# Kernel tuning notes

Measured on AMD Instinct MI355X. Metric: run time of the kernel, lower is better.

The kernel has to match this reference:

```python
import jax, jax.numpy as jnp
import numpy as np

EMBED = 512
HEADS = 8
HEAD_DIM = EMBED // HEADS
LN_EPS = 1e-5


def setup_inputs() -> dict:
    key = jax.random.key(0)
    ks = jax.random.split(key, 13)
    B, L = 4, 2048
    s = 1.0 / np.sqrt(EMBED)
    inp = {
        "values": jax.random.normal(ks[0], (B, L, EMBED), dtype=jnp.float32),
        "keys": jax.random.normal(ks[1], (B, L, EMBED), dtype=jnp.float32),
        "query": jax.random.normal(ks[2], (B, L, EMBED), dtype=jnp.float32),
        "Wq": jax.random.uniform(ks[3], (EMBED, EMBED), jnp.float32, -s, s),
        "bq": jax.random.uniform(ks[4], (EMBED,), jnp.float32, -s, s),
        "Wk": jax.random.uniform(ks[5], (EMBED, EMBED), jnp.float32, -s, s),
        "bk": jax.random.uniform(ks[6], (EMBED,), jnp.float32, -s, s),
        "Wv": jax.random.uniform(ks[7], (EMBED, EMBED), jnp.float32, -s, s),
        "bv": jax.random.uniform(ks[8], (EMBED,), jnp.float32, -s, s),
        "Wo": jax.random.uniform(ks[9], (EMBED, EMBED), jnp.float32, -s, s),
        "bo": jax.random.uniform(ks[10], (EMBED,), jnp.float32, -s, s),
        "ln_g": jnp.ones((EMBED,), jnp.float32),
        "ln_b": jnp.zeros((EMBED,), jnp.float32),
    }
    return inp


def reference(values, keys, query, Wq, bq, Wk, bk, Wv, bv, Wo, bo, ln_g, ln_b):
    B, L, _ = query.shape
    # separate QKV linears (torch Linear: x @ W^T + b)
    Q = (query @ Wq.T + bq).reshape(B, L, HEADS, HEAD_DIM)
    K = (keys @ Wk.T + bk).reshape(B, L, HEADS, HEAD_DIM)
    V = (values @ Wv.T + bv).reshape(B, L, HEADS, HEAD_DIM)
    # explicit QK^T scores: [B, H, Q, K]
    scores = jnp.einsum("nqhd,nkhd->nhqk", Q, K) / np.sqrt(HEAD_DIM)
    attn = jax.nn.softmax(scores, axis=-1)
    out = jnp.einsum("nhqk,nkhd->nqhd", attn, V).reshape(B, L, EMBED)
    out = out @ Wo.T + bo
    # residual + LayerNorm (dropout = identity in eval)
    x = out + query
    mu = jnp.mean(x, axis=-1, keepdims=True)
    var = jnp.var(x, axis=-1, keepdims=True)
    return (x - mu) * jax.lax.rsqrt(var + LN_EPS) * ln_g + ln_b
```

## Files before the change

kernel.cpp:

```cpp
#include <hip/hip_runtime.h>

typedef short bf16x8 __attribute__((ext_vector_type(8)));
typedef short s16x4 __attribute__((ext_vector_type(4)));
typedef float f32x4 __attribute__((ext_vector_type(4)));
typedef unsigned int uint4v __attribute__((ext_vector_type(4)));
typedef unsigned int uint2v __attribute__((ext_vector_type(2)));

#define BLM   8192
#define EMB   512
#define LSEQ  2048
#define NHEAD 8
#define HDIM  64

typedef __attribute__((address_space(3))) char lds_ch;

__device__ __forceinline__ unsigned short f2bf(float x) {
    unsigned int u = __builtin_bit_cast(unsigned int, x);
    u += 0x7FFFu + ((u >> 16) & 1u);
    return (unsigned short)(u >> 16);
}

__device__ __forceinline__ unsigned int cvtpk(float lo, float hi) {
    unsigned int r;
    asm("v_cvt_pk_bf16_f32 %0, %1, %2" : "=v"(r) : "v"(lo), "v"(hi));
    return r;
}

__device__ __forceinline__ int swz(int row, int bcol) {
    return row * 128 + (bcol ^ ((row & 7) << 4));
}

#define GLL16(g, l) __builtin_amdgcn_global_load_lds( \
    (const __attribute__((address_space(1))) void*)(g), \
    (__attribute__((address_space(3))) void*)(l), 16, 0, 0)

#define TR16(dst, a, OFF) asm volatile("ds_read_b64_tr_b16 %0, %1 offset:%2" \
    : "=v"(dst) : "v"(a), "n"(OFF))

__global__ __launch_bounds__(256, 3) void k_gemm_qkv(
    const float* __restrict__ Xq, const float* __restrict__ Xk, const float* __restrict__ Xv,
    const float* __restrict__ Wq, const float* __restrict__ Wk, const float* __restrict__ Wv,
    const float* __restrict__ bq, const float* __restrict__ bk, const float* __restrict__ bv,
    unsigned short* __restrict__ Qb, unsigned short* __restrict__ Kb, unsigned short* __restrict__ Vb)
{
    const int z = blockIdx.z;
    const float* X    = (z == 0) ? Xq : (z == 1) ? Xk : Xv;
    const float* W    = (z == 0) ? Wq : (z == 1) ? Wk : Wv;
    const float* bias = (z == 0) ? bq : (z == 1) ? bk : bv;
    unsigned short* out = (z == 0) ? Qb : (z == 1) ? Kb : Vb;
    const float osc = (z == 0) ? 0.125f * 1.44269504088896340736f : 1.0f;

    __shared__ __align__(16) char lds[32768];
    char* As = lds;
    char* Bs = lds + 16384;

    const int tid  = threadIdx.x;
    const int lane = tid & 63;
    const int wave = tid >> 6;
    const int wm = wave >> 1, wn = wave & 1;
    const int lr = lane & 15, lk = lane >> 4;
    const int m0 = blockIdx.x * 128, n0 = blockIdx.y * 128;

    f32x4 acc[4][4] = {};

    const float* pa = X + (size_t)(m0 + (tid >> 4)) * EMB + (tid & 15) * 4;
    const float* pb = W + (size_t)(n0 + (tid >> 4)) * EMB + (tid & 15) * 4;

    float4 ar[8], br[8];
    #pragma unroll
    for (int i = 0; i < 8; ++i) {
        ar[i] = *(const float4*)(pa + (size_t)i * 16 * EMB);
        br[i] = *(const float4*)(pb + (size_t)i * 16 * EMB);
    }
    pa += 64; pb += 64;

    for (int kt = 0; kt < 8; ++kt) {
        __syncthreads();
        #pragma unroll
        for (int i = 0; i < 8; ++i) {
            int f = tid + i * 256;
            int r = f >> 4, c4 = f & 15;
            uint2v p; p.x = cvtpk(ar[i].x, ar[i].y); p.y = cvtpk(ar[i].z, ar[i].w);
            *(uint2v*)(As + swz(r, c4 * 8)) = p;
            uint2v q; q.x = cvtpk(br[i].x, br[i].y); q.y = cvtpk(br[i].z, br[i].w);
            *(uint2v*)(Bs + swz(r, c4 * 8)) = q;
        }
        if (kt < 7) {
            #pragma unroll
            for (int i = 0; i < 8; ++i) {
                ar[i] = *(const float4*)(pa + (size_t)i * 16 * EMB);
                br[i] = *(const float4*)(pb + (size_t)i * 16 * EMB);
            }
            pa += 64; pb += 64;
        }
        __syncthreads();
        #pragma unroll
        for (int ks = 0; ks < 2; ++ks) {
            bf16x8 af[4], bfr[4];
            #pragma unroll
            for (int fm = 0; fm < 4; ++fm)
                af[fm] = *(const bf16x8*)(As + swz(wm * 64 + fm * 16 + lr, ks * 64 + lk * 16));
            #pragma unroll
            for (int fn = 0; fn < 4; ++fn)
                bfr[fn] = *(const bf16x8*)(Bs + swz(wn * 64 + fn * 16 + lr, ks * 64 + lk * 16));
            #pragma unroll
            for (int fm = 0; fm < 4; ++fm)
                #pragma unroll
                for (int fn = 0; fn < 4; ++fn)
                    acc[fm][fn] = __builtin_amdgcn_mfma_f32_16x16x32_bf16(af[fm], bfr[fn], acc[fm][fn], 0, 0, 0);
        }
    }
    #pragma unroll
    for (int fn = 0; fn < 4; ++fn) {
        int n = n0 + wn * 64 + fn * 16 + lr;
        float bv_ = bias[n];
        #pragma unroll
        for (int fm = 0; fm < 4; ++fm) {
            int mb = m0 + wm * 64 + fm * 16 + lk * 4;
            #pragma unroll
            for (int j = 0; j < 4; ++j)
                out[(size_t)(mb + j) * EMB + n] = f2bf((acc[fm][fn][j] + bv_) * osc);
        }
    }
}

__global__ __launch_bounds__(256, 3) void k_gemm_out(
    const unsigned short* __restrict__ AO, const float* __restrict__ Wo,
    const float* __restrict__ bo, const float* __restrict__ res,
    float* __restrict__ Xout)
{
    __shared__ __align__(16) char lds[32768];
    char* As = lds;
    char* Bs = lds + 16384;

    const int tid  = threadIdx.x;
    const int lane = tid & 63;
    const int wave = tid >> 6;
    const int wm = wave >> 1, wn = wave & 1;
    const int lr = lane & 15, lk = lane >> 4;
    const int m0 = blockIdx.x * 128, n0 = blockIdx.y * 128;

    f32x4 acc[4][4] = {};

    const unsigned short* pA = AO + (size_t)(m0 + (tid >> 3)) * EMB + (tid & 7) * 8;
    const float* pB = Wo + (size_t)(n0 + (tid >> 4)) * EMB + (tid & 15) * 4;

    uint4v arA[4]; float4 brB[8];
    #pragma unroll
    for (int i = 0; i < 4; ++i) arA[i] = *(const uint4v*)(pA + (size_t)i * 32 * EMB);
    #pragma unroll
    for (int i = 0; i < 8; ++i) brB[i] = *(const float4*)(pB + (size_t)i * 16 * EMB);
    pA += 64; pB += 64;

    for (int kt = 0; kt < 8; ++kt) {
        __syncthreads();
        #pragma unroll
        for (int i = 0; i < 4; ++i) {
            int f = tid + i * 256;
            int r = f >> 3, c8 = f & 7;
            *(uint4v*)(As + swz(r, c8 * 16)) = arA[i];
        }
        #pragma unroll
        for (int i = 0; i < 8; ++i) {
            int f = tid + i * 256;
            int r = f >> 4, c4 = f & 15;
            uint2v q; q.x = cvtpk(brB[i].x, brB[i].y); q.y = cvtpk(brB[i].z, brB[i].w);
            *(uint2v*)(Bs + swz(r, c4 * 8)) = q;
        }
        if (kt < 7) {
            #pragma unroll
            for (int i = 0; i < 4; ++i) arA[i] = *(const uint4v*)(pA + (size_t)i * 32 * EMB);
            #pragma unroll
            for (int i = 0; i < 8; ++i) brB[i] = *(const float4*)(pB + (size_t)i * 16 * EMB);
            pA += 64; pB += 64;
        }
        __syncthreads();
        #pragma unroll
        for (int ks = 0; ks < 2; ++ks) {
            bf16x8 af[4], bfr[4];
            #pragma unroll
            for (int fm = 0; fm < 4; ++fm)
                af[fm] = *(const bf16x8*)(As + swz(wm * 64 + fm * 16 + lr, ks * 64 + lk * 16));
            #pragma unroll
            for (int fn = 0; fn < 4; ++fn)
                bfr[fn] = *(const bf16x8*)(Bs + swz(wn * 64 + fn * 16 + lr, ks * 64 + lk * 16));
            #pragma unroll
            for (int fm = 0; fm < 4; ++fm)
                #pragma unroll
                for (int fn = 0; fn < 4; ++fn)
                    acc[fm][fn] = __builtin_amdgcn_mfma_f32_16x16x32_bf16(af[fm], bfr[fn], acc[fm][fn], 0, 0, 0);
        }
    }
    #pragma unroll
    for (int fn = 0; fn < 4; ++fn) {
        int n = n0 + wn * 64 + fn * 16 + lr;
        float bv_ = bo[n];
        #pragma unroll
        for (int fm = 0; fm < 4; ++fm) {
            int mb = m0 + wm * 64 + fm * 16 + lk * 4;
            #pragma unroll
            for (int j = 0; j < 4; ++j) {
                size_t idx = (size_t)(mb + j) * EMB + n;
                Xout[idx] = acc[fm][fn][j] + bv_ + res[idx];
            }
        }
    }
}

__global__ __launch_bounds__(256, 4) void k_attn(
    const unsigned short* __restrict__ Qb, const unsigned short* __restrict__ Kb,
    const unsigned short* __restrict__ Vb, unsigned short* __restrict__ AO)
{
    __shared__ __align__(16) char lds[32768];
    lds_ch* LB = (lds_ch*)lds;

    const int tid  = threadIdx.x;
    const int lane = tid & 63;
    const int wave = tid >> 6;
    const int lr = lane & 15, lk = lane >> 4;

    const int bid  = blockIdx.x;
    const int orig = (bid & 7) * 64 + (bid >> 3);
    const int qx = orig & 15, bh = orig >> 4;
    const int b = bh >> 3, h = bh & 7;
    const size_t base = (size_t)b * LSEQ * EMB + h * HDIM;
    const int q0 = qx * 128 + wave * 32;

    const int c0 = tid, c1 = tid + 256;
    auto kcol = [](int c) { int r = c >> 3; return ((c & 7) * 8) ^ ((r & 7) * 8); };
    const unsigned short* srcK0 = Kb + base + (size_t)(c0 >> 3) * EMB + kcol(c0);
    const unsigned short* srcK1 = Kb + base + (size_t)(c1 >> 3) * EMB + kcol(c1);
    auto vsrc = [&](int c) {
        int kv = ((c >> 3) & 15) * 4 + ((c >> 1) & 3);
        int d  = (c >> 7) * 16 + (c & 1) * 8;
        return Vb + base + (size_t)kv * EMB + d;
    };
    const unsigned short* srcV0 = vsrc(c0);
    const unsigned short* srcV1 = vsrc(c1);

    auto stage = [&](int par) {
        lds_ch* kd = LB + par * 8192 + wave * 1024;
        lds_ch* vd = LB + 16384 + par * 8192 + wave * 1024;
        GLL16(srcK0, kd);
        GLL16(srcK1, kd + 4096);
        GLL16(srcV0, vd);
        GLL16(srcV1, vd + 4096);
        srcK0 += 64 * EMB; srcK1 += 64 * EMB;
        srcV0 += 64 * EMB; srcV1 += 64 * EMB;
    };

    bf16x8 qf[2][2];
    #pragma unroll
    for (int qg = 0; qg < 2; ++qg)
        #pragma unroll
        for (int ks = 0; ks < 2; ++ks)
            qf[qg][ks] = *(const bf16x8*)(Qb + base + (size_t)(q0 + qg * 16 + lr) * EMB + ks * 32 + lk * 8);

    f32x4 oaccT[2][4] = {};
    float lrow[2] = {0.f, 0.f};

    lds_ch* vadB = LB + 16384 + lk * 128 + lr * 2;

    stage(0);

    for (int t = 0; t < 32; ++t) {
        const int par = t & 1;
        __syncthreads();
        if (t < 31) stage(par ^ 1);

        char* Kl = lds + par * 8192;
        f32x4 s0[4] = {}, s1[4] = {};
        __builtin_amdgcn_s_setprio(1);
        #pragma unroll
        for (int ks = 0; ks < 2; ++ks) {
            bf16x8 kf[4];
            #pragma unroll
            for (int blk = 0; blk < 4; ++blk)
                kf[blk] = *(const bf16x8*)(Kl + swz(blk * 16 + lr, ks * 64 + lk * 16));
            #pragma unroll
            for (int blk = 0; blk < 4; ++blk) {
                s0[blk] = __builtin_amdgcn_mfma_f32_16x16x32_bf16(kf[blk], qf[0][ks], s0[blk], 0, 0, 0);
                s1[blk] = __builtin_amdgcn_mfma_f32_16x16x32_bf16(kf[blk], qf[1][ks], s1[blk], 0, 0, 0);
            }
        }
        __builtin_amdgcn_s_setprio(0);

        #pragma unroll
        for (int blk = 0; blk < 4; ++blk)
            #pragma unroll
            for (int j = 0; j < 4; ++j) {
                s0[blk][j] = __builtin_amdgcn_exp2f(s0[blk][j]);
                s1[blk][j] = __builtin_amdgcn_exp2f(s1[blk][j]);
            }
        {
            f32x4 pc = (s0[0] + s0[1]) + (s0[2] + s0[3]);
            lrow[0] += (pc[0] + pc[1]) + (pc[2] + pc[3]);
            f32x4 qc = (s1[0] + s1[1]) + (s1[2] + s1[3]);
            lrow[1] += (qc[0] + qc[1]) + (qc[2] + qc[3]);
        }

        bf16x8 pf0[2], pf1[2];
        #pragma unroll
        for (int k = 0; k < 2; ++k) {
            uint4v w;
            w.x = cvtpk(s0[2 * k][0],     s0[2 * k][1]);
            w.y = cvtpk(s0[2 * k][2],     s0[2 * k][3]);
            w.z = cvtpk(s0[2 * k + 1][0], s0[2 * k + 1][1]);
            w.w = cvtpk(s0[2 * k + 1][2], s0[2 * k + 1][3]);
            pf0[k] = __builtin_bit_cast(bf16x8, w);
            uint4v v;
            v.x = cvtpk(s1[2 * k][0],     s1[2 * k][1]);
            v.y = cvtpk(s1[2 * k][2],     s1[2 * k][3]);
            v.z = cvtpk(s1[2 * k + 1][0], s1[2 * k + 1][1]);
            v.w = cvtpk(s1[2 * k + 1][2], s1[2 * k + 1][3]);
            pf1[k] = __builtin_bit_cast(bf16x8, v);
        }

        lds_ch* vad = vadB + par * 8192;
        __builtin_amdgcn_s_setprio(1);
        #pragma unroll
        for (int fd = 0; fd < 4; ++fd) {
            uint2v t0, t1, t2, t3;
            TR16(t0, vad, 0);    TR16(t1, vad, 512);
            TR16(t2, vad, 1024); TR16(t3, vad, 1536);
            asm volatile("s_waitcnt lgkmcnt(0)" ::: "memory");
            __builtin_amdgcn_sched_barrier(0);
            uint4v w0; w0.x = t0.x; w0.y = t0.y; w0.z = t1.x; w0.w = t1.y;
            uint4v w1; w1.x = t2.x; w1.y = t2.y; w1.z = t3.x; w1.w = t3.y;
            bf16x8 v0 = __builtin_bit_cast(bf16x8, w0);
            bf16x8 v1 = __builtin_bit_cast(bf16x8, w1);
            oaccT[0][fd] = __builtin_amdgcn_mfma_f32_16x16x32_bf16(v0, pf0[0], oaccT[0][fd], 0, 0, 0);
            oaccT[1][fd] = __builtin_amdgcn_mfma_f32_16x16x32_bf16(v0, pf1[0], oaccT[1][fd], 0, 0, 0);
            oaccT[0][fd] = __builtin_amdgcn_mfma_f32_16x16x32_bf16(v1, pf0[1], oaccT[0][fd], 0, 0, 0);
            oaccT[1][fd] = __builtin_amdgcn_mfma_f32_16x16x32_bf16(v1, pf1[1], oaccT[1][fd], 0, 0, 0);
            vad += 2048;
        }
        __builtin_amdgcn_s_setprio(0);
    }

    #pragma unroll
    for (int qg = 0; qg < 2; ++qg) {
        float lr_ = lrow[qg];
        lr_ += __shfl_xor(lr_, 16);
        lr_ += __shfl_xor(lr_, 32);
        float inv = 1.f / lr_;
        unsigned short* aorow = AO + base + (size_t)(q0 + qg * 16 + lr) * EMB;
        #pragma unroll
        for (int fd = 0; fd < 4; ++fd) {
            s16x4 s;
            #pragma unroll
            for (int j = 0; j < 4; ++j) s[j] = (short)f2bf(oaccT[qg][fd][j] * inv);
            *(s16x4*)(aorow + fd * 16 + lk * 4) = s;
        }
    }
}

__global__ __launch_bounds__(64) void k_ln(
    const float* __restrict__ X, const float* __restrict__ g,
    const float* __restrict__ bta, float* __restrict__ out)
{
    const int row = blockIdx.x, lane = threadIdx.x;
    const float* x = X + (size_t)row * EMB;
    float4 a = *(const float4*)(x + lane * 8);
    float4 c = *(const float4*)(x + lane * 8 + 4);
    float s  = a.x + a.y + a.z + a.w + c.x + c.y + c.z + c.w;
    float sq = a.x*a.x + a.y*a.y + a.z*a.z + a.w*a.w + c.x*c.x + c.y*c.y + c.z*c.z + c.w*c.w;
    #pragma unroll
    for (int msk = 1; msk < 64; msk <<= 1) { s += __shfl_xor(s, msk); sq += __shfl_xor(sq, msk); }
    float mu  = s * (1.f / 512.f);
    float var = sq * (1.f / 512.f) - mu * mu;
    float rs  = rsqrtf(var + 1e-5f);
    float4 g0 = *(const float4*)(g + lane * 8), g1 = *(const float4*)(g + lane * 8 + 4);
    float4 b0 = *(const float4*)(bta + lane * 8), b1 = *(const float4*)(bta + lane * 8 + 4);
    float4 o0, o1;
    o0.x = (a.x - mu) * rs * g0.x + b0.x;  o0.y = (a.y - mu) * rs * g0.y + b0.y;
    o0.z = (a.z - mu) * rs * g0.z + b0.z;  o0.w = (a.w - mu) * rs * g0.w + b0.w;
    o1.x = (c.x - mu) * rs * g1.x + b1.x;  o1.y = (c.y - mu) * rs * g1.y + b1.y;
    o1.z = (c.z - mu) * rs * g1.z + b1.z;  o1.w = (c.w - mu) * rs * g1.w + b1.w;
    *(float4*)(out + (size_t)row * EMB + lane * 8) = o0;
    *(float4*)(out + (size_t)row * EMB + lane * 8 + 4) = o1;
}

extern "C" void kernel_launch(void* const* d_in, const int* in_sizes, int n_in,
                              void* d_out, int out_size, void* d_ws, size_t ws_size,
                              hipStream_t stream) {
    const float* values = (const float*)d_in[0];
    const float* keys   = (const float*)d_in[1];
    const float* query  = (const float*)d_in[2];
    const float* Wq = (const float*)d_in[3];  const float* bq = (const float*)d_in[4];
    const float* Wk = (const float*)d_in[5];  const float* bk = (const float*)d_in[6];
    const float* Wv = (const float*)d_in[7];  const float* bv = (const float*)d_in[8];
    const float* Wo = (const float*)d_in[9];  const float* bo = (const float*)d_in[10];
    const float* lng = (const float*)d_in[11];
    const float* lnb = (const float*)d_in[12];

    char* ws = (char*)d_ws;
    unsigned short* Qb = (unsigned short*)(ws);
    unsigned short* Kb = (unsigned short*)(ws + 8u  * 1024 * 1024);
    unsigned short* Vb = (unsigned short*)(ws + 16u * 1024 * 1024);
    unsigned short* AO = (unsigned short*)(ws + 24u * 1024 * 1024);
    float*          Xr = (float*)(ws);

    dim3 gqkv(64, 4, 3);
    k_gemm_qkv<<<gqkv, 256, 0, stream>>>(query, keys, values, Wq, Wk, Wv, bq, bk, bv, Qb, Kb, Vb);
    k_attn<<<512, 256, 0, stream>>>(Qb, Kb, Vb, AO);
    k_gemm_out<<<dim3(64, 4), 256, 0, stream>>>(AO, Wo, bo, query, Xr);
    k_ln<<<8192, 64, 0, stream>>>(Xr, lng, lnb, (float*)d_out);
}
```

Baseline: 88.11 us.

## Split KV tile across wave pairs in attention and reduce partials via LDS

```diff
diff --git a/kernel.cpp b/kernel.cpp
--- a/kernel.cpp
+++ b/kernel.cpp
@@ -13,6 +13,7 @@
 #define HDIM  64
 
 typedef __attribute__((address_space(3))) char lds_ch;
+typedef __attribute__((address_space(3))) float lds_f32;
 
 __device__ __forceinline__ unsigned short f2bf(float x) {
     unsigned int u = __builtin_bit_cast(unsigned int, x);
@@ -217,14 +218,16 @@
     const int tid  = threadIdx.x;
     const int lane = tid & 63;
     const int wave = tid >> 6;
+    const int qh   = wave & 1;
+    const int kvh  = wave >> 1;
     const int lr = lane & 15, lk = lane >> 4;
 
     const int bid  = blockIdx.x;
-    const int orig = (bid & 7) * 64 + (bid >> 3);
-    const int qx = orig & 15, bh = orig >> 4;
+    const int orig = (bid & 7) * 128 + (bid >> 3);
+    const int qx = orig & 31, bh = orig >> 5;
     const int b = bh >> 3, h = bh & 7;
     const size_t base = (size_t)b * LSEQ * EMB + h * HDIM;
-    const int q0 = qx * 128 + wave * 32;
+    const int q0 = qx * 64 + qh * 32;
 
     const int c0 = tid, c1 = tid + 256;
     auto kcol = [](int c) { int r = c >> 3; return ((c & 7) * 8) ^ ((r & 7) * 8); };
@@ -259,7 +262,7 @@
     f32x4 oaccT[2][4] = {};
     float lrow[2] = {0.f, 0.f};
 
-    lds_ch* vadB = LB + 16384 + lk * 128 + lr * 2;
+    lds_ch* vadB = LB + 16384 + kvh * 1024 + lk * 128 + lr * 2;
 
     stage(0);
 
@@ -269,88 +272,98 @@
         if (t < 31) stage(par ^ 1);
 
         char* Kl = lds + par * 8192;
-        f32x4 s0[4] = {}, s1[4] = {};
+        f32x4 s0[2] = {}, s1[2] = {};
         __builtin_amdgcn_s_setprio(1);
         #pragma unroll
         for (int ks = 0; ks < 2; ++ks) {
-            bf16x8 kf[4];
-            #pragma unroll
-            for (int blk = 0; blk < 4; ++blk)
-                kf[blk] = *(const bf16x8*)(Kl + swz(blk * 16 + lr, ks * 64 + lk * 16));
-            #pragma unroll
-            for (int blk = 0; blk < 4; ++blk) {
-                s0[blk] = __builtin_amdgcn_mfma_f32_16x16x32_bf16(kf[blk], qf[0][ks], s0[blk], 0, 0, 0);
-                s1[blk] = __builtin_amdgcn_mfma_f32_16x16x32_bf16(kf[blk], qf[1][ks], s1[blk], 0, 0, 0);
-            }
+            bf16x8 kf0 = *(const bf16x8*)(Kl + swz((kvh * 2 + 0) * 16 + lr, ks * 64 + lk * 16));
+            bf16x8 kf1 = *(const bf16x8*)(Kl + swz((kvh * 2 + 1) * 16 + lr, ks * 64 + lk * 16));
+            s0[0] = __builtin_amdgcn_mfma_f32_16x16x32_bf16(kf0, qf[0][ks], s0[0], 0, 0, 0);
+            s1[0] = __builtin_amdgcn_mfma_f32_16x16x32_bf16(kf0, qf[1][ks], s1[0], 0, 0, 0);
+            s0[1] = __builtin_amdgcn_mfma_f32_16x16x32_bf16(kf1, qf[0][ks], s0[1], 0, 0, 0);
+            s1[1] = __builtin_amdgcn_mfma_f32_16x16x32_bf16(kf1, qf[1][ks], s1[1], 0, 0, 0);
         }
         __builtin_amdgcn_s_setprio(0);
 
         #pragma unroll
-        for (int blk = 0; blk < 4; ++blk)
+        for (int blk = 0; blk < 2; ++blk)
             #pragma unroll
             for (int j = 0; j < 4; ++j) {
                 s0[blk][j] = __builtin_amdgcn_exp2f(s0[blk][j]);
                 s1[blk][j] = __builtin_amdgcn_exp2f(s1[blk][j]);
             }
         {
-            f32x4 pc = (s0[0] + s0[1]) + (s0[2] + s0[3]);
+            f32x4 pc = s0[0] + s0[1];
             lrow[0] += (pc[0] + pc[1]) + (pc[2] + pc[3]);
-            f32x4 qc = (s1[0] + s1[1]) + (s1[2] + s1[3]);
+            f32x4 qc = s1[0] + s1[1];
             lrow[1] += (qc[0] + qc[1]) + (qc[2] + qc[3]);
         }
 
-        bf16x8 pf0[2], pf1[2];
-        #pragma unroll
-        for (int k = 0; k < 2; ++k) {
-            uint4v w;
-            w.x = cvtpk(s0[2 * k][0],     s0[2 * k][1]);
-            w.y = cvtpk(s0[2 * k][2],     s0[2 * k][3]);
-            w.z = cvtpk(s0[2 * k + 1][0], s0[2 * k + 1][1]);
-            w.w = cvtpk(s0[2 * k + 1][2], s0[2 * k + 1][3]);
-            pf0[k] = __builtin_bit_cast(bf16x8, w);
-            uint4v v;
-            v.x = cvtpk(s1[2 * k][0],     s1[2 * k][1]);
-            v.y = cvtpk(s1[2 * k][2],     s1[2 * k][3]);
-            v.z = cvtpk(s1[2 * k + 1][0], s1[2 * k + 1][1]);
-            v.w = cvtpk(s1[2 * k + 1][2], s1[2 * k + 1][3]);
-            pf1[k] = __builtin_bit_cast(bf16x8, v);
-        }
+        uint4v w;
+        w.x = cvtpk(s0[0][0], s0[0][1]); w.y = cvtpk(s0[0][2], s0[0][3]);
+        w.z = cvtpk(s0[1][0], s0[1][1]); w.w = cvtpk(s0[1][2], s0[1][3]);
+        bf16x8 pf0 = __builtin_bit_cast(bf16x8, w);
+        uint4v v;
+        v.x = cvtpk(s1[0][0], s1[0][1]); v.y = cvtpk(s1[0][2], s1[0][3]);
+        v.z = cvtpk(s1[1][0], s1[1][1]); v.w = cvtpk(s1[1][2], s1[1][3]);
+        bf16x8 pf1 = __builtin_bit_cast(bf16x8, v);
 
         lds_ch* vad = vadB + par * 8192;
         __builtin_amdgcn_s_setprio(1);
         #pragma unroll
         for (int fd = 0; fd < 4; ++fd) {
-            uint2v t0, t1, t2, t3;
-            TR16(t0, vad, 0);    TR16(t1, vad, 512);
-            TR16(t2, vad, 1024); TR16(t3, vad, 1536);
+            uint2v ta, tb;
+            TR16(ta, vad, 0); TR16(tb, vad, 512);
             asm volatile("s_waitcnt lgkmcnt(0)" ::: "memory");
             __builtin_amdgcn_sched_barrier(0);
-            uint4v w0; w0.x = t0.x; w0.y = t0.y; w0.z = t1.x; w0.w = t1.y;
-            uint4v w1; w1.x = t2.x; w1.y = t2.y; w1.z = t3.x; w1.w = t3.y;
-            bf16x8 v0 = __builtin_bit_cast(bf16x8, w0);
-            bf16x8 v1 = __builtin_bit_cast(bf16x8, w1);
-            oaccT[0][fd] = __builtin_amdgcn_mfma_f32_16x16x32_bf16(v0, pf0[0], oaccT[0][fd], 0, 0, 0);
-            oaccT[1][fd] = __builtin_amdgcn_mfma_f32_16x16x32_bf16(v0, pf1[0], oaccT[1][fd], 0, 0, 0);
-            oaccT[0][fd] = __builtin_amdgcn_mfma_f32_16x16x32_bf16(v1, pf0[1], oaccT[0][fd], 0, 0, 0);
-            oaccT[1][fd] = __builtin_amdgcn_mfma_f32_16x16x32_bf16(v1, pf1[1], oaccT[1][fd], 0, 0, 0);
+            uint4v wv; wv.x = ta.x; wv.y = ta.y; wv.z = tb.x; wv.w = tb.y;
+            bf16x8 vf = __builtin_bit_cast(bf16x8, wv);
+            oaccT[0][fd] = __builtin_amdgcn_mfma_f32_16x16x32_bf16(vf, pf0, oaccT[0][fd], 0, 0, 0);
+            oaccT[1][fd] = __builtin_amdgcn_mfma_f32_16x16x32_bf16(vf, pf1, oaccT[1][fd], 0, 0, 0);
             vad += 2048;
         }
         __builtin_amdgcn_s_setprio(0);
     }
 
-    #pragma unroll
-    for (int qg = 0; qg < 2; ++qg) {
-        float lr_ = lrow[qg];
-        lr_ += __shfl_xor(lr_, 16);
-        lr_ += __shfl_xor(lr_, 32);
-        float inv = 1.f / lr_;
-        unsigned short* aorow = AO + base + (size_t)(q0 + qg * 16 + lr) * EMB;
-        #pragma unroll
-        for (int fd = 0; fd < 4; ++fd) {
-            s16x4 s;
-            #pragma unroll
-            for (int j = 0; j < 4; ++j) s[j] = (short)f2bf(oaccT[qg][fd][j] * inv);
-            *(s16x4*)(aorow + fd * 16 + lk * 4) = s;
+    __syncthreads();
+    lds_f32* red = (lds_f32*)LB;
+    if (kvh == 1) {
+        lds_f32* dst = red + (qh * 64 + lane) * 34;
+        #pragma unroll
+        for (int qg = 0; qg < 2; ++qg)
+            #pragma unroll
+            for (int fd = 0; fd < 4; ++fd)
+                #pragma unroll
+                for (int j = 0; j < 4; ++j)
+                    dst[qg * 16 + fd * 4 + j] = oaccT[qg][fd][j];
+        dst[32] = lrow[0]; dst[33] = lrow[1];
+    }
+    __syncthreads();
+    if (kvh == 0) {
+        const lds_f32* src = red + (qh * 64 + lane) * 34;
+        #pragma unroll
+        for (int qg = 0; qg < 2; ++qg)
+            #pragma unroll
+            for (int fd = 0; fd < 4; ++fd)
+                #pragma unroll
+                for (int j = 0; j < 4; ++j)
+                    oaccT[qg][fd][j] += src[qg * 16 + fd * 4 + j];
+        lrow[0] += src[32]; lrow[1] += src[33];
+
+        #pragma unroll
+        for (int qg = 0; qg < 2; ++qg) {
+            float lr_ = lrow[qg];
+            lr_ += __shfl_xor(lr_, 16);
+            lr_ += __shfl_xor(lr_, 32);
+            float inv = 1.f / lr_;
+            unsigned short* aorow = AO + base + (size_t)(q0 + qg * 16 + lr) * EMB;
+            #pragma unroll
+            for (int fd = 0; fd < 4; ++fd) {
+                s16x4 s;
+                #pragma unroll
+                for (int j = 0; j < 4; ++j) s[j] = (short)f2bf(oaccT[qg][fd][j] * inv);
+                *(s16x4*)(aorow + fd * 16 + lk * 4) = s;
+            }
         }
     }
 }
@@ -403,7 +416,7 @@
 
     dim3 gqkv(64, 4, 3);
     k_gemm_qkv<<<gqkv, 256, 0, stream>>>(query, keys, values, Wq, Wk, Wv, bq, bk, bv, Qb, Kb, Vb);
-    k_attn<<<512, 256, 0, stream>>>(Qb, Kb, Vb, AO);
+    k_attn<<<1024, 256, 0, stream>>>(Qb, Kb, Vb, AO);
     k_gemm_out<<<dim3(64, 4), 256, 0, stream>>>(AO, Wo, bo, query, Xr);
     k_ln<<<8192, 64, 0, stream>>>(Xr, lng, lnb, (float*)d_out);
 }
```

New measurement: 90.48 us. 2.7% more time.
